# Kernel tuning notes

Measured on AMD Instinct MI355X. Metric: run time of the kernel, lower is better.

## Reference

```python
import jax, jax.numpy as jnp
import numpy as np

G, KP, EPS = 4, 9, 1e-5  # deformable groups, 3x3 kernel points, BN eps


def setup_inputs() -> dict:
    key = jax.random.key(0)
    ks = jax.random.split(key, 16)
    N, C1, C2, H, W = 8, 256, 256, 64, 64
    c = int(C1 * 1.0) // 16 * 16  # 256 internal width
    OM = int(np.ceil(G * KP * 3 / 8) * 8)  # 112 padded offset/mask dim (108 used)
    sd = 0.02
    return {
        "x": jax.random.normal(ks[0], (N, C1, H, W), jnp.float32),
        "cv1_w": jax.random.normal(ks[1], (c, C1), jnp.float32) * sd,
        "cv1_b": jax.random.normal(ks[2], (c,), jnp.float32) * sd,
        "value_w": jax.random.normal(ks[3], (c, c), jnp.float32) * sd,
        "value_b": jax.random.normal(ks[4], (c,), jnp.float32) * sd,
        "dw_w": jax.random.normal(ks[5], (c,), jnp.float32) * sd + 1.0,
        "dw_b": jax.random.normal(ks[6], (c,), jnp.float32) * sd,
        "om_w": jax.random.normal(ks[7], (OM, c), jnp.float32) * sd,
        "om_b": jax.random.normal(ks[8], (OM,), jnp.float32) * sd,
        "out_w": jax.random.normal(ks[9], (c, c), jnp.float32) * sd,
        "cv2_w": jax.random.normal(ks[10], (C2, c), jnp.float32) * sd,
        "bn_gamma": jnp.ones((C2,), jnp.float32),
        "bn_beta": jnp.zeros((C2,), jnp.float32),
        "bn_mean": jax.random.normal(ks[11], (C2,), jnp.float32) * 0.1,
        "bn_var": jax.random.uniform(ks[12], (C2,), jnp.float32, minval=0.5, maxval=1.5),
    }


def _dcnv4(value, offset_mask, H, W):
    """DCNv4 core: offset-based bilinear sampling + unnormalized-mask aggregation.
    value: (N,H,W,c) NHWC features; offset_mask: (N,H,W,OM), per group layout
    [2*KP offsets (dx,dy pairs), KP masks]; no softmax on masks (DCNv4)."""
    N, c = value.shape[0], value.shape[-1]
    GC = c // G
    om = offset_mask[..., : G * KP * 3].reshape(N, H, W, G, 3 * KP)
    offs = om[..., : 2 * KP].reshape(N, H, W, G, KP, 2)  # (dx, dy), x = width axis
    mask = om[..., 2 * KP:]                               # (N,H,W,G,KP)
    ky, kx = jnp.meshgrid(jnp.arange(-1, 2, dtype=jnp.float32),
                          jnp.arange(-1, 2, dtype=jnp.float32), indexing="ij")
    kx, ky = kx.reshape(KP), ky.reshape(KP)               # 3x3 dilation-1 grid
    base_x = jnp.arange(W, dtype=jnp.float32)[None, None, :, None, None]
    base_y = jnp.arange(H, dtype=jnp.float32)[None, :, None, None, None]
    px = base_x + kx + offs[..., 0]                       # (N,H,W,G,KP) abs pixel x
    py = base_y + ky + offs[..., 1]
    x0, y0 = jnp.floor(px), jnp.floor(py)
    fx, fy = px - x0, py - y0
    x0i, y0i = x0.astype(jnp.int32), y0.astype(jnp.int32)
    vflat = value.reshape(N, H * W, G, GC).transpose(0, 2, 1, 3)  # (N,G,L,GC)
    acc = jnp.zeros((N, G, H, W, KP, GC), value.dtype)
    for dy, dx, wgt in ((0, 0, (1 - fy) * (1 - fx)), (0, 1, (1 - fy) * fx),
                        (1, 0, fy * (1 - fx)), (1, 1, fy * fx)):
        yy, xx = y0i + dy, x0i + dx
        valid = (yy >= 0) & (yy < H) & (xx >= 0) & (xx < W)   # zero padding
        idx = jnp.clip(yy, 0, H - 1) * W + jnp.clip(xx, 0, W - 1)
        idx_g = idx.transpose(0, 3, 1, 2, 4).reshape(N, G, H * W * KP)
        smp = jnp.take_along_axis(vflat, idx_g[..., None], axis=2)
        smp = smp.reshape(N, G, H, W, KP, GC)
        acc = acc + smp * (wgt * valid).transpose(0, 3, 1, 2, 4)[..., None]
    out = (acc * mask.transpose(0, 3, 1, 2, 4)[..., None]).sum(axis=4)  # (N,G,H,W,GC)
    return out.transpose(0, 2, 3, 1, 4).reshape(N, H, W, c)


def reference(x, cv1_w, cv1_b, value_w, value_b, dw_w, dw_b, om_w, om_b,
              out_w, cv2_w, bn_gamma, bn_beta, bn_mean, bn_var):
    N, C1, H, W = x.shape
    t = jnp.einsum("nchw,dc->nhwd", x, cv1_w) + cv1_b       # cv1 1x1 conv -> NHWC
    value = t @ value_w.T + value_b                          # DCNv4 value_proj
    om = (t * dw_w + dw_b) @ om_w.T + om_b                   # depthwise 1x1 + linear
    y = _dcnv4(value, om, H, W)
    y = y @ out_w.T                                          # output_proj (no bias)
    y = jnp.einsum("nhwc,dc->nhwd", y, cv2_w)                # cv2 1x1 (no bias)
    y = (y - bn_mean) * bn_gamma * jax.lax.rsqrt(bn_var + EPS) + bn_beta  # BN (eval)
    y = y * jax.nn.sigmoid(y)                                # SiLU
    return y.transpose(0, 3, 1, 2)                           # back to NCHW
```

## Files before the change

### kernel.cpp

```cpp
#include <hip/hip_runtime.h>
#include <hip/hip_bf16.h>
#include <math.h>

#define NN    8
#define HH    64
#define WW    64
#define HW    4096
#define NHW   32768
#define DALL  384
#define EPSBN 1e-5f

typedef __attribute__((ext_vector_type(8))) short short8v;
typedef __attribute__((ext_vector_type(4))) float f32x4;
typedef __attribute__((ext_vector_type(2))) float f32x2;

__device__ __forceinline__ float b2f(unsigned short u) {
    union { unsigned int i; float f; } v; v.i = ((unsigned int)u) << 16; return v.f;
}
__device__ __forceinline__ unsigned short f2b(float f) {
    __hip_bfloat16 h = __float2bfloat16(f);
    return *reinterpret_cast<const unsigned short*>(&h);
}
__device__ __forceinline__ f32x2 bf2x(int u) {
    union { int i; float f; } a, b;
    a.i = u << 16;
    b.i = u & 0xffff0000;
    f32x2 r; r[0] = a.f; r[1] = b.f; return r;
}


__global__ __launch_bounds__(256)
void prep_kernel(const float* __restrict__ cv1_w, const float* __restrict__ cv1_b,
                 const float* __restrict__ value_w, const float* __restrict__ value_b,
                 const float* __restrict__ dw_w, const float* __restrict__ dw_b,
                 const float* __restrict__ om_w, const float* __restrict__ om_b,
                 const float* __restrict__ out_w, const float* __restrict__ cv2_w,
                 const float* __restrict__ bn_g, const float* __restrict__ bn_b,
                 const float* __restrict__ bn_m, const float* __restrict__ bn_v,
                 unsigned short* __restrict__ Wallbf, float* __restrict__ ball,
                 unsigned short* __restrict__ Woutbf, float* __restrict__ bout)
{
    int job = blockIdx.x * 256 + threadIdx.x;
    if (job < 65536) {
        int d = job >> 8, cc = job & 255;
        float s0=0.f, s1=0.f, s2=0.f, s3=0.f;
        for (int e = 0; e < 256; e += 4) {
            float4 wv = *reinterpret_cast<const float4*>(&value_w[d*256+e]);
            s0 = fmaf(wv.x, cv1_w[(e+0)*256+cc], s0);
            s1 = fmaf(wv.y, cv1_w[(e+1)*256+cc], s1);
            s2 = fmaf(wv.z, cv1_w[(e+2)*256+cc], s2);
            s3 = fmaf(wv.w, cv1_w[(e+3)*256+cc], s3);
        }
        Wallbf[job] = f2b((s0+s1)+(s2+s3));
    } else if (job < 94208) {
        int idx = job - 65536;
        int o = idx >> 8, cc = idx & 255;
        float s0=0.f, s1=0.f, s2=0.f, s3=0.f;
        for (int e = 0; e < 256; e += 4) {
            float4 wv = *reinterpret_cast<const float4*>(&om_w[o*256+e]);
            float4 dv = *reinterpret_cast<const float4*>(&dw_w[e]);
            s0 = fmaf(wv.x*dv.x, cv1_w[(e+0)*256+cc], s0);
            s1 = fmaf(wv.y*dv.y, cv1_w[(e+1)*256+cc], s1);
            s2 = fmaf(wv.z*dv.z, cv1_w[(e+2)*256+cc], s2);
            s3 = fmaf(wv.w*dv.w, cv1_w[(e+3)*256+cc], s3);
        }
        Wallbf[job] = f2b((s0+s1)+(s2+s3));
    } else if (job < 98304) {
        Wallbf[job] = 0;
    } else if (job < 163840) {
        int idx = job - 98304;
        int d = idx >> 8, cc = idx & 255;
        float s0=0.f, s1=0.f, s2=0.f, s3=0.f;
        for (int e = 0; e < 256; e += 4) {
            float4 wv = *reinterpret_cast<const float4*>(&cv2_w[d*256+e]);
            s0 = fmaf(wv.x, out_w[(e+0)*256+cc], s0);
            s1 = fmaf(wv.y, out_w[(e+1)*256+cc], s1);
            s2 = fmaf(wv.z, out_w[(e+2)*256+cc], s2);
            s3 = fmaf(wv.w, out_w[(e+3)*256+cc], s3);
        }
        float sc = bn_g[d] * rsqrtf(bn_v[d] + EPSBN);
        Woutbf[idx] = f2b(((s0+s1)+(s2+s3)) * sc);
    } else if (job < 164096) {
        int d = job - 163840;
        float s = value_b[d];
        for (int e = 0; e < 256; ++e) s = fmaf(value_w[d*256+e], cv1_b[e], s);
        ball[d] = s;
    } else if (job < 164208) {
        int o = job - 164096;
        float s = om_b[o];
        for (int e = 0; e < 256; ++e)
            s = fmaf(om_w[o*256+e], fmaf(dw_w[e], cv1_b[e], dw_b[e]), s);
        ball[256 + o] = s;
    } else if (job < 164224) {
        ball[368 + job - 164208] = 0.f;
    } else if (job < 164480) {
        int d = job - 164224;
        float sc = bn_g[d] * rsqrtf(bn_v[d] + EPSBN);
        bout[d] = fmaf(-bn_m[d], sc, bn_b[d]);
    }
}

__global__ __launch_bounds__(256)
void gemm_vo_kernel(const float* __restrict__ x, const unsigned short* __restrict__ Wallbf,
                    const float* __restrict__ ball, unsigned short* __restrict__ VO)
{
    __shared__ unsigned short As[8192];
    __shared__ unsigned short Bs[8192];
    int t = threadIdx.x;
    int m0 = blockIdx.y * 128;
    int n0 = blockIdx.x * 128;
    int nimg = m0 >> 12, hw0 = m0 & 4095;
    int lane = t & 63;
    int wv = t >> 6;
    int wr = wv >> 1, wc = wv & 1;
    int r_l = lane & 15, kg_l = lane >> 4;
    int ci = t >> 6;
    int l  = t & 63;

    const float* xbase = x + (size_t)(nimg * 256) * 4096 + hw0;

    f32x4 acc[4][4] = {};

    for (int kt = 0; kt < 4; ++kt) {
        int c0 = kt * 64;
        float2 val[16];
        #pragma unroll
        for (int i = 0; i < 16; ++i)
            val[i] = *reinterpret_cast<const float2*>(
                &xbase[(size_t)(c0 + ci*16 + i) * 4096 + 2*l]);
        __syncthreads();
        #pragma unroll
        for (int rsel = 0; rsel < 2; ++rsel) {
            int row = 2*l + rsel;
            #pragma unroll
            for (int kgi = 0; kgi < 2; ++kgi) {
                int kg = ci*2 + kgi;
                short8v s;
                #pragma unroll
                for (int j = 0; j < 8; ++j)
                    s[j] = (short)f2b(rsel ? val[kgi*8+j].y : val[kgi*8+j].x);
                *reinterpret_cast<short8v*>(&As[row*64 + ((kg ^ (row & 7)) << 3)]) = s;
            }
        }
        #pragma unroll
        for (int i = 0; i < 4; ++i) {
            int idx = t + i*256;
            int row = idx >> 3, kg = idx & 7;
            *reinterpret_cast<short8v*>(&Bs[row*64 + ((kg ^ (row & 7)) << 3)]) =
                *reinterpret_cast<const short8v*>(&Wallbf[(size_t)(n0 + row)*256 + c0 + kg*8]);
        }
        __syncthreads();
        #pragma unroll
        for (int ks = 0; ks < 2; ++ks) {
            short8v af[4], bfr[4];
            #pragma unroll
            for (int m = 0; m < 4; ++m) {
                int row = wr*64 + m*16 + r_l;
                af[m] = *reinterpret_cast<const short8v*>(
                    &As[row*64 + (((ks*4 + kg_l) ^ (row & 7)) << 3)]);
            }
            #pragma unroll
            for (int n = 0; n < 4; ++n) {
                int row = wc*64 + n*16 + r_l;
                bfr[n] = *reinterpret_cast<const short8v*>(
                    &Bs[row*64 + (((ks*4 + kg_l) ^ (row & 7)) << 3)]);
            }
            #pragma unroll
            for (int m = 0; m < 4; ++m)
                #pragma unroll
                for (int n = 0; n < 4; ++n)
                    acc[m][n] = __builtin_amdgcn_mfma_f32_16x16x32_bf16(af[m], bfr[n], acc[m][n], 0, 0, 0);
        }
    }

    #pragma unroll
    for (int n = 0; n < 4; ++n) {
        int d = n0 + wc*64 + n*16 + r_l;
        float bb = ball[d];
        #pragma unroll
        for (int m = 0; m < 4; ++m) {
            int pr = m0 + wr*64 + m*16 + (kg_l << 2);
            #pragma unroll
            for (int r = 0; r < 4; ++r)
                VO[(size_t)(pr + r)*384 + d] = f2b(acc[m][n][r] + bb);
        }
    }
}

__global__ __launch_bounds__(512, 4)
void dcn_gemm_kernel(const unsigned short* __restrict__ VO,
                     const unsigned short* __restrict__ Woutbf,
                     const float* __restrict__ bout, float* __restrict__ out)
{
    __shared__ unsigned short y_lds[16384];
    __shared__ char u_buf[32768];
    float* om_s = reinterpret_cast<float*>(u_buf);
    unsigned short* As = reinterpret_cast<unsigned short*>(u_buf);

    int t = threadIdx.x;
    int bid = blockIdx.x;
    int logical = ((bid & 7) << 6) + (bid >> 3);
    int p0 = logical * 64;
    int nimg = p0 >> 12;
    int hw0 = p0 & 4095;
    int h = hw0 >> 6;

    const unsigned short* vimg = VO + (size_t)nimg * (HW * (size_t)DALL);

    for (int i = t; i < 6912; i += 512) {
        int pl = i / 108, j = i - pl * 108;
        om_s[pl * 108 + j] = b2f(vimg[(size_t)(hw0 + pl) * DALL + 256 + j]);
    }
    __syncthreads();

    int ch8 = t & 7;
    #pragma unroll
    for (int iter = 0; iter < 4; ++iter) {
        int slotIdx = iter * 64 + (t >> 3);
        int px = slotIdx >> 2, g = slotIdx & 3;
        int w = px;
        const unsigned short* vbase = vimg + g*64 + ch8*8;
        const float* o = om_s + px*108 + g*27;

        f32x2 acc2[4] = {};
        #pragma unroll
        for (int k = 0; k < 9; ++k) {
            float dxo = o[2*k], dyo = o[2*k+1], m = o[18+k];
            float pxf = (float)(w + (k % 3) - 1) + dxo;
            float pyf = (float)(h + (k / 3) - 1) + dyo;
            float x0f = floorf(pxf), y0f = floorf(pyf);
            float fx = pxf - x0f, fy = pyf - y0f;
            int x0 = (int)x0f, y0 = (int)y0f;
            #pragma unroll
            for (int dyy = 0; dyy < 2; ++dyy) {
                #pragma unroll
                for (int dxx = 0; dxx < 2; ++dxx) {
                    int yy = y0 + dyy, xx = x0 + dxx;
                    bool valid = (yy >= 0) & (yy < HH) & (xx >= 0) & (xx < WW);
                    float wgt = (dyy ? fy : 1.f - fy) * (dxx ? fx : 1.f - fx);
                    float wmc = valid ? (m * wgt) : 0.f;
                    int yc = min(max(yy, 0), HH - 1);
                    int xc = min(max(xx, 0), WW - 1);
                    int4 v = *reinterpret_cast<const int4*>(
                        &vbase[((yc << 6) + xc) * DALL]);
                    f32x2 wm2; wm2[0] = wmc; wm2[1] = wmc;
                    int vv[4] = {v.x, v.y, v.z, v.w};
                    #pragma unroll
                    for (int q = 0; q < 4; ++q)
                        acc2[q] += bf2x(vv[q]) * wm2;
                }
            }
        }
        short8v ov;
        #pragma unroll
        for (int q = 0; q < 4; ++q) {
            ov[2*q]   = (short)f2b(acc2[q][0]);
            ov[2*q+1] = (short)f2b(acc2[q][1]);
        }
        *reinterpret_cast<short8v*>(
            &y_lds[g*4096 + px*64 + ((ch8 ^ (px & 7)) << 3)]) = ov;
    }

    int lane = t & 63;
    int wv = t >> 6;
    int wr = wv >> 1, wc = wv & 1;
    int r_l = lane & 15, kg_l = lane >> 4;

    f32x4 acc[4][2] = {};
    for (int kt = 0; kt < 4; ++kt) {
        int c0 = kt * 64;
        __syncthreads();
        #pragma unroll
        for (int i = 0; i < 4; ++i) {
            int idx = t + i * 512;
            int row = idx >> 3, kg = idx & 7;
            *reinterpret_cast<short8v*>(&As[row*64 + ((kg ^ (row & 7)) << 3)]) =
                *reinterpret_cast<const short8v*>(&Woutbf[(size_t)row*256 + c0 + kg*8]);
        }
        __syncthreads();
        __builtin_amdgcn_s_setprio(1);
        #pragma unroll
        for (int ks = 0; ks < 2; ++ks) {
            short8v af[4], bfr[2];
            #pragma unroll
            for (int m = 0; m < 4; ++m) {
                int row = wr*64 + m*16 + r_l;
                af[m] = *reinterpret_cast<const short8v*>(
                    &As[row*64 + (((ks*4 + kg_l) ^ (row & 7)) << 3)]);
            }
            #pragma unroll
            for (int n = 0; n < 2; ++n) {
                int row = wc*32 + n*16 + r_l;
                bfr[n] = *reinterpret_cast<const short8v*>(
                    &y_lds[kt*4096 + row*64 + (((ks*4 + kg_l) ^ (row & 7)) << 3)]);
            }
            #pragma unroll
            for (int m = 0; m < 4; ++m)
                #pragma unroll
                for (int n = 0; n < 2; ++n)
                    acc[m][n] = __builtin_amdgcn_mfma_f32_16x16x32_bf16(af[m], bfr[n], acc[m][n], 0, 0, 0);
        }
        __builtin_amdgcn_s_setprio(0);
    }

    #pragma unroll
    for (int m = 0; m < 4; ++m) {
        int dbase = wr*64 + m*16 + (kg_l << 2);
        #pragma unroll
        for (int r = 0; r < 4; ++r) {
            int d = dbase + r;
            float bb = bout[d];
            #pragma unroll
            for (int n = 0; n < 2; ++n) {
                int pcol = wc*32 + n*16 + r_l;
                float z = acc[m][n][r] + bb;
                float sv = z / (1.f + __expf(-z));
                out[((size_t)(nimg*256 + d))*4096 + hw0 + pcol] = sv;
            }
        }
    }
}

extern "C" void kernel_launch(void* const* d_in, const int* in_sizes, int n_in,
                              void* d_out, int out_size, void* d_ws, size_t ws_size,
                              hipStream_t stream) {
    const float* x       = (const float*)d_in[0];
    const float* cv1_w   = (const float*)d_in[1];
    const float* cv1_b   = (const float*)d_in[2];
    const float* value_w = (const float*)d_in[3];
    const float* value_b = (const float*)d_in[4];
    const float* dw_w    = (const float*)d_in[5];
    const float* dw_b    = (const float*)d_in[6];
    const float* om_w    = (const float*)d_in[7];
    const float* om_b    = (const float*)d_in[8];
    const float* out_w   = (const float*)d_in[9];
    const float* cv2_w   = (const float*)d_in[10];
    const float* bn_g    = (const float*)d_in[11];
    const float* bn_b    = (const float*)d_in[12];
    const float* bn_m    = (const float*)d_in[13];
    const float* bn_v    = (const float*)d_in[14];

    char* ws = (char*)d_ws;
    unsigned short* VO     = (unsigned short*)(ws);
    unsigned short* Wallbf = (unsigned short*)(ws + 25165824);
    unsigned short* Woutbf = (unsigned short*)(ws + 25362432);
    float*          ball   = (float*)(ws + 25493504);
    float*          bout   = (float*)(ws + 25495040);
    float* out = (float*)d_out;

    prep_kernel<<<643, 256, 0, stream>>>(cv1_w, cv1_b, value_w, value_b, dw_w, dw_b,
                                         om_w, om_b, out_w, cv2_w,
                                         bn_g, bn_b, bn_m, bn_v,
                                         Wallbf, ball, Woutbf, bout);
    gemm_vo_kernel<<<dim3(3, 256), 256, 0, stream>>>(x, Wallbf, ball, VO);
    dcn_gemm_kernel<<<512, 512, 0, stream>>>(VO, Woutbf, bout, out);
}
```

Before: 89.16 us.

## Interleave per-group deformable sampling with output-proj GEMM k-tiles

Moves the bilinear deformable sampling for each group inside the GEMM k-loop, so group g's sampling runs in the same phase as the weight-tile load for k-tile g. The intent is to let the global gathers for sampling overlap the weight staging and the MFMA work of neighbouring waves. It also keeps the offset/mask staging in bf16 and loads it with 16-byte vector loads instead of scalar bf16-to-float conversions. The cost is that the separate LDS buffers (As no longer aliases om_s) raise shared-memory use, which may reduce occupancy, and a second barrier per iteration is added.

New measurement: 99.42 us. 1.12x slower.

```diff
diff --git a/kernel.cpp b/kernel.cpp
--- a/kernel.cpp
+++ b/kernel.cpp
@@ -193,9 +193,8 @@
                      const float* __restrict__ bout, float* __restrict__ out)
 {
     __shared__ unsigned short y_lds[16384];
-    __shared__ char u_buf[32768];
-    float* om_s = reinterpret_cast<float*>(u_buf);
-    unsigned short* As = reinterpret_cast<unsigned short*>(u_buf);
+    __shared__ unsigned short As[16384];
+    __shared__ unsigned short om_s[64 * 112];
 
     int t = threadIdx.x;
     int bid = blockIdx.x;
@@ -207,69 +206,23 @@
 
     const unsigned short* vimg = VO + (size_t)nimg * (HW * (size_t)DALL);
 
-    for (int i = t; i < 6912; i += 512) {
-        int pl = i / 108, j = i - pl * 108;
-        om_s[pl * 108 + j] = b2f(vimg[(size_t)(hw0 + pl) * DALL + 256 + j]);
+    for (int i = t; i < 896; i += 512) {
+        int row = i / 14, c8 = i - row * 14;
+        *reinterpret_cast<short8v*>(&om_s[row * 112 + c8 * 8]) =
+            *reinterpret_cast<const short8v*>(&vimg[(size_t)(hw0 + row) * DALL + 256 + c8 * 8]);
     }
     __syncthreads();
-
-    int ch8 = t & 7;
-    #pragma unroll
-    for (int iter = 0; iter < 4; ++iter) {
-        int slotIdx = iter * 64 + (t >> 3);
-        int px = slotIdx >> 2, g = slotIdx & 3;
-        int w = px;
-        const unsigned short* vbase = vimg + g*64 + ch8*8;
-        const float* o = om_s + px*108 + g*27;
-
-        f32x2 acc2[4] = {};
-        #pragma unroll
-        for (int k = 0; k < 9; ++k) {
-            float dxo = o[2*k], dyo = o[2*k+1], m = o[18+k];
-            float pxf = (float)(w + (k % 3) - 1) + dxo;
-            float pyf = (float)(h + (k / 3) - 1) + dyo;
-            float x0f = floorf(pxf), y0f = floorf(pyf);
-            float fx = pxf - x0f, fy = pyf - y0f;
-            int x0 = (int)x0f, y0 = (int)y0f;
-            #pragma unroll
-            for (int dyy = 0; dyy < 2; ++dyy) {
-                #pragma unroll
-                for (int dxx = 0; dxx < 2; ++dxx) {
-                    int yy = y0 + dyy, xx = x0 + dxx;
-                    bool valid = (yy >= 0) & (yy < HH) & (xx >= 0) & (xx < WW);
-                    float wgt = (dyy ? fy : 1.f - fy) * (dxx ? fx : 1.f - fx);
-                    float wmc = valid ? (m * wgt) : 0.f;
-                    int yc = min(max(yy, 0), HH - 1);
-                    int xc = min(max(xx, 0), WW - 1);
-                    int4 v = *reinterpret_cast<const int4*>(
-                        &vbase[((yc << 6) + xc) * DALL]);
-                    f32x2 wm2; wm2[0] = wmc; wm2[1] = wmc;
-                    int vv[4] = {v.x, v.y, v.z, v.w};
-                    #pragma unroll
-                    for (int q = 0; q < 4; ++q)
-                        acc2[q] += bf2x(vv[q]) * wm2;
-                }
-            }
-        }
-        short8v ov;
-        #pragma unroll
-        for (int q = 0; q < 4; ++q) {
-            ov[2*q]   = (short)f2b(acc2[q][0]);
-            ov[2*q+1] = (short)f2b(acc2[q][1]);
-        }
-        *reinterpret_cast<short8v*>(
-            &y_lds[g*4096 + px*64 + ((ch8 ^ (px & 7)) << 3)]) = ov;
-    }
 
     int lane = t & 63;
     int wv = t >> 6;
     int wr = wv >> 1, wc = wv & 1;
     int r_l = lane & 15, kg_l = lane >> 4;
+    int px_d = t >> 3, ch8 = t & 7;
 
     f32x4 acc[4][2] = {};
-    for (int kt = 0; kt < 4; ++kt) {
-        int c0 = kt * 64;
-        __syncthreads();
+
+    for (int g = 0; g < 4; ++g) {
+        int c0 = g * 64;
         #pragma unroll
         for (int i = 0; i < 4; ++i) {
             int idx = t + i * 512;
@@ -277,7 +230,53 @@
             *reinterpret_cast<short8v*>(&As[row*64 + ((kg ^ (row & 7)) << 3)]) =
                 *reinterpret_cast<const short8v*>(&Woutbf[(size_t)row*256 + c0 + kg*8]);
         }
+
+        {
+            int w = px_d;
+            const unsigned short* vbase = vimg + g*64 + ch8*8;
+            const unsigned short* o = om_s + px_d*112 + g*27;
+
+            f32x2 acc2[4] = {};
+            #pragma unroll
+            for (int k = 0; k < 9; ++k) {
+                float dxo = b2f(o[2*k]), dyo = b2f(o[2*k+1]), m = b2f(o[18+k]);
+                float pxf = (float)(w + (k % 3) - 1) + dxo;
+                float pyf = (float)(h + (k / 3) - 1) + dyo;
+                float x0f = floorf(pxf), y0f = floorf(pyf);
+                float fx = pxf - x0f, fy = pyf - y0f;
+                int x0 = (int)x0f, y0 = (int)y0f;
+                #pragma unroll
+                for (int dyy = 0; dyy < 2; ++dyy) {
+                    #pragma unroll
+                    for (int dxx = 0; dxx < 2; ++dxx) {
+                        int yy = y0 + dyy, xx = x0 + dxx;
+                        bool valid = (yy >= 0) & (yy < HH) & (xx >= 0) & (xx < WW);
+                        float wgt = (dyy ? fy : 1.f - fy) * (dxx ? fx : 1.f - fx);
+                        float wmc = valid ? (m * wgt) : 0.f;
+                        int yc = min(max(yy, 0), HH - 1);
+                        int xc = min(max(xx, 0), WW - 1);
+                        int4 v = *reinterpret_cast<const int4*>(
+                            &vbase[((yc << 6) + xc) * DALL]);
+                        f32x2 wm2; wm2[0] = wmc; wm2[1] = wmc;
+                        int vv[4] = {v.x, v.y, v.z, v.w};
+                        #pragma unroll
+                        for (int q = 0; q < 4; ++q)
+                            acc2[q] += bf2x(vv[q]) * wm2;
+                    }
+                }
+            }
+            short8v ov;
+            #pragma unroll
+            for (int q = 0; q < 4; ++q) {
+                ov[2*q]   = (short)f2b(acc2[q][0]);
+                ov[2*q+1] = (short)f2b(acc2[q][1]);
+            }
+            *reinterpret_cast<short8v*>(
+                &y_lds[g*4096 + px_d*64 + ((ch8 ^ (px_d & 7)) << 3)]) = ov;
+        }
+
         __syncthreads();
+
         __builtin_amdgcn_s_setprio(1);
         #pragma unroll
         for (int ks = 0; ks < 2; ++ks) {
@@ -292,7 +291,7 @@
             for (int n = 0; n < 2; ++n) {
                 int row = wc*32 + n*16 + r_l;
                 bfr[n] = *reinterpret_cast<const short8v*>(
-                    &y_lds[kt*4096 + row*64 + (((ks*4 + kg_l) ^ (row & 7)) << 3)]);
+                    &y_lds[g*4096 + row*64 + (((ks*4 + kg_l) ^ (row & 7)) << 3)]);
             }
             #pragma unroll
             for (int m = 0; m < 4; ++m)
@@ -301,6 +300,8 @@
                     acc[m][n] = __builtin_amdgcn_mfma_f32_16x16x32_bf16(af[m], bfr[n], acc[m][n], 0, 0, 0);
         }
         __builtin_amdgcn_s_setprio(0);
+
+        __syncthreads();
     }
 
     #pragma unroll
```
